# Kernel tuning notes

Hardware: AMD Instinct MI355X
Metric: run time of the kernel (lower is better)

## Reference

```python
import jax, jax.numpy as jnp
import numpy as np

D_MODEL = 1024
NUM_HEADS = 16
HEAD_DIM = D_MODEL // NUM_HEADS
SEQ_LEN = 2048
THETA = 10000.0


def setup_inputs() -> dict:
    key = jax.random.key(0)
    ks = jax.random.split(key, 9)
    s = 1.0 / np.sqrt(D_MODEL)
    inp = {
        "x": jax.random.normal(ks[0], (2, SEQ_LEN, D_MODEL), dtype=jnp.float32),
        "Wq": jax.random.uniform(ks[1], (D_MODEL, D_MODEL), jnp.float32, -s, s),
        "bq": jax.random.uniform(ks[2], (D_MODEL,), jnp.float32, -s, s),
        "Wk": jax.random.uniform(ks[3], (D_MODEL, D_MODEL), jnp.float32, -s, s),
        "bk": jax.random.uniform(ks[4], (D_MODEL,), jnp.float32, -s, s),
        "Wv": jax.random.uniform(ks[5], (D_MODEL, D_MODEL), jnp.float32, -s, s),
        "bv": jax.random.uniform(ks[6], (D_MODEL,), jnp.float32, -s, s),
        "Wo": jax.random.uniform(ks[7], (D_MODEL, D_MODEL), jnp.float32, -s, s),
        "bo": jax.random.uniform(ks[8], (D_MODEL,), jnp.float32, -s, s),
    }
    return inp


def _rope_cos_sin(seq_len, dim, theta):
    inv_freq = 1.0 / theta ** (jnp.arange(0, dim, 2, dtype=jnp.float32) / dim)  # [dim/2]
    t = jnp.arange(seq_len, dtype=jnp.float32)
    freqs = jnp.outer(t, inv_freq)  # [S, dim/2]
    return jnp.cos(freqs), jnp.sin(freqs)


def _apply_rope(x, cos, sin):
    # x: [B, H, S, head_dim]; interleaved complex pairs (even, odd)
    x2 = x.reshape(*x.shape[:-1], -1, 2)  # [B,H,S,hd/2,2]
    xe, xo = x2[..., 0], x2[..., 1]
    c = cos[None, None, :, :]
    s = sin[None, None, :, :]
    oe = xe * c - xo * s
    oo = xe * s + xo * c
    return jnp.stack([oe, oo], axis=-1).reshape(x.shape)


def reference(x, Wq, bq, Wk, bk, Wv, bv, Wo, bo):
    B, S, D = x.shape
    H, hd = NUM_HEADS, HEAD_DIM
    q = x @ Wq.T + bq
    k = x @ Wk.T + bk
    v = x @ Wv.T + bv
    # [B, H, S, hd]
    q = q.reshape(B, S, H, hd).transpose(0, 2, 1, 3)
    k = k.reshape(B, S, H, hd).transpose(0, 2, 1, 3)
    v = v.reshape(B, S, H, hd).transpose(0, 2, 1, 3)
    cos, sin = _rope_cos_sin(S, hd, THETA)
    q = _apply_rope(q, cos, sin)
    k = _apply_rope(k, cos, sin)
    scores = jnp.einsum("bhqd,bhkd->bhqk", q, k) / jnp.sqrt(jnp.float32(hd))
    causal = jnp.triu(jnp.ones((S, S), dtype=bool), k=1)
    scores = jnp.where(causal[None, None, :, :], -jnp.inf, scores)
    attn = jax.nn.softmax(scores, axis=-1)
    out = jnp.einsum("bhqk,bhkd->bhqd", attn, v)
    out = out.transpose(0, 2, 1, 3).reshape(B, S, D)
    return out @ Wo.T + bo
```

## Files before the change

### kernel.cpp

```cpp
#include <hip/hip_runtime.h>
#include <hip/hip_bf16.h>

#define S_LEN 2048
#define DM 1024
#define NH 16
#define HD 64
#define M_ROWS 4096
#define LOG2E 1.4426950408889634f
#define MASKVAL -1.0e4f
#define QSCALE 0.18033688011112042f

typedef __attribute__((ext_vector_type(8))) short short8;
typedef __attribute__((ext_vector_type(2))) float f32x2;
typedef __attribute__((ext_vector_type(4))) float f32x4;
typedef __attribute__((ext_vector_type(16))) float f32x16;

__device__ inline ushort f2b(float f) {
  union { float f; unsigned u; } v; v.f = f;
  unsigned r = v.u + 0x7fffu + ((v.u >> 16) & 1u);
  return (ushort)(r >> 16);
}

__device__ inline float b2f(ushort u) {
  union { unsigned u; float f; } v; v.u = ((unsigned)u) << 16; return v.f;
}

__device__ inline unsigned pk_bf16(float a, float b) {
  __hip_bfloat162 h = __float22bfloat162_rn(make_float2(a, b));
  union { __hip_bfloat162 h; unsigned u; } v; v.h = h;
  return v.u;
}

__device__ inline float fexp2(float x) { return __builtin_amdgcn_exp2f(x); }

__device__ inline void gl_lds16(const void* g, void* l) {
  __builtin_amdgcn_global_load_lds(
      (const __attribute__((address_space(1))) void*)g,
      (__attribute__((address_space(3))) void*)l, 16, 0, 0);
}

__global__ __launch_bounds__(256) void cast_rope_kernel(
    const float* __restrict__ x, const float* __restrict__ Wq, const float* __restrict__ Wk,
    const float* __restrict__ Wv, const float* __restrict__ Wo,
    ushort* __restrict__ xb, ushort* __restrict__ Wqb, ushort* __restrict__ Wkb,
    ushort* __restrict__ Wvb, ushort* __restrict__ Wob,
    float* __restrict__ ropeC, float* __restrict__ ropeS) {
  const int bid = blockIdx.x;
  if (bid >= 8192) {
    int idx = (bid - 8192) * 256 + threadIdx.x;
    int s = idx >> 5, i = idx & 31;
    float inv = exp2f(-(float)i * (13.287712379549449f / 32.0f));
    float a = (float)s * inv;
    ropeC[idx] = cosf(a);
    ropeS[idx] = sinf(a);
    return;
  }
  int i = bid * 256 + threadIdx.x;
  int r = i >> 18, off = i & 0x3FFFF;
  const float4* s;
  uint2* d;
  switch (r) {
    case 0: case 1: case 2: case 3: s = (const float4*)x + i;  d = (uint2*)xb + i;  break;
    case 4: s = (const float4*)Wq + off; d = (uint2*)Wqb + off; break;
    case 5: s = (const float4*)Wk + off; d = (uint2*)Wkb + off; break;
    case 6: s = (const float4*)Wv + off; d = (uint2*)Wvb + off; break;
    default: s = (const float4*)Wo + off; d = (uint2*)Wob + off; break;
  }
  float4 v = *s;
  uint2 o;
  o.x = pk_bf16(v.x, v.y);
  o.y = pk_bf16(v.z, v.w);
  *d = o;
}

__global__ __launch_bounds__(256) void gemm_qkv_kernel(const ushort* __restrict__ xb,
    const ushort* __restrict__ Wqb, const ushort* __restrict__ Wkb, const ushort* __restrict__ Wvb,
    const float* __restrict__ bq, const float* __restrict__ bk, const float* __restrict__ bv,
    const float* __restrict__ ropeC, const float* __restrict__ ropeS,
    ushort* __restrict__ qb, ushort* __restrict__ kb, ushort* __restrict__ vT) {
  __shared__ ushort lds[17408];
  ushort* As = lds;
  ushort* Bs = lds + 8192;
  const int z = blockIdx.z;
  const ushort* W = (z == 0) ? Wqb : ((z == 1) ? Wkb : Wvb);
  const float* bias = (z == 0) ? bq : ((z == 1) ? bk : bv);
  const int m0 = blockIdx.x * 128, n0 = blockIdx.y * 128;
  const int t = threadIdx.x, lane = t & 63, wave = t >> 6;
  const int wr = (wave >> 1) * 64, wc = (wave & 1) * 64;
  const int lr = lane & 15, lg = lane >> 4;

  const int slot0 = wave * 128 + lane, slot1 = slot0 + 64;
  const int row0 = slot0 >> 2, g0 = (slot0 & 3) ^ (row0 & 3);
  const int row1 = slot1 >> 2, g1 = (slot1 & 3) ^ (row1 & 3);
  const ushort* Ap0 = &xb[(size_t)(m0 + row0) * DM + g0 * 8];
  const ushort* Ap1 = &xb[(size_t)(m0 + row1) * DM + g1 * 8];
  const ushort* Wp0 = &W[(size_t)(n0 + row0) * DM + g0 * 8];
  const ushort* Wp1 = &W[(size_t)(n0 + row1) * DM + g1 * 8];

  f32x4 acc[4][4];
#pragma unroll
  for (int a = 0; a < 4; a++)
#pragma unroll
    for (int b = 0; b < 4; b++) acc[a][b] = (f32x4){0.f, 0.f, 0.f, 0.f};

  gl_lds16(Ap0, &As[slot0 * 8]);
  gl_lds16(Ap1, &As[slot1 * 8]);
  gl_lds16(Wp0, &Bs[slot0 * 8]);
  gl_lds16(Wp1, &Bs[slot1 * 8]);
  __syncthreads();

  int buf = 0;
  for (int i = 0; i < 32; i++) {
    if (i + 1 < 32) {
      const int k0 = (i + 1) * 32;
      const int bo = (buf ^ 1) * 4096;
      gl_lds16(Ap0 + k0, &As[bo + slot0 * 8]);
      gl_lds16(Ap1 + k0, &As[bo + slot1 * 8]);
      gl_lds16(Wp0 + k0, &Bs[bo + slot0 * 8]);
      gl_lds16(Wp1 + k0, &Bs[bo + slot1 * 8]);
    }
    const int fb = buf * 4096;
    short8 af[4], bf[4];
#pragma unroll
    for (int mt = 0; mt < 4; mt++) {
      const int row = wr + mt * 16 + lr;
      af[mt] = *(const short8*)&As[fb + (row * 4 + (lg ^ (row & 3))) * 8];
    }
#pragma unroll
    for (int nt = 0; nt < 4; nt++) {
      const int row = wc + nt * 16 + lr;
      bf[nt] = *(const short8*)&Bs[fb + (row * 4 + (lg ^ (row & 3))) * 8];
    }
#pragma unroll
    for (int mt = 0; mt < 4; mt++)
#pragma unroll
      for (int nt = 0; nt < 4; nt++)
        acc[mt][nt] = __builtin_amdgcn_mfma_f32_16x16x32_bf16(af[mt], bf[nt], acc[mt][nt], 0, 0, 0);
    __syncthreads();
    buf ^= 1;
  }

#pragma unroll
  for (int mt = 0; mt < 4; mt++) {
#pragma unroll
    for (int nt = 0; nt < 4; nt++) {
      const int nloc = wc + nt * 16 + lr;
      const float bn = bias[n0 + nloc];
#pragma unroll
      for (int r = 0; r < 4; r++) {
        const int mloc = wr + mt * 16 + lg * 4 + r;
        const ushort v = f2b(acc[mt][nt][r] + bn);
        if (z < 2) lds[mloc * 136 + nloc] = v;
        else       lds[nloc * 136 + mloc] = v;
      }
    }
  }
  __syncthreads();

  const int b = m0 >> 11;
  if (z < 2) {
    ushort* dst = (z == 0) ? qb : kb;
    const float qscale = (z == 0) ? QSCALE : 1.0f;
#pragma unroll
    for (int c = 0; c < 8; c++) {
      const int sloc = c * 16 + (t >> 4);
      const int nloc = (t & 15) * 8;
      short8 val = *(const short8*)&lds[sloc * 136 + nloc];
      const int s = (m0 + sloc) & (S_LEN - 1);
      const int h = (n0 + nloc) >> 6;
      const int d0 = nloc & 63;
      const float4 cv = *(const float4*)&ropeC[s * 32 + d0 / 2];
      const float4 sv = *(const float4*)&ropeS[s * 32 + d0 / 2];
      uint4 o;
      {
        float e = b2f((ushort)val[0]), od = b2f((ushort)val[1]);
        o.x = pk_bf16((e * cv.x - od * sv.x) * qscale, (e * sv.x + od * cv.x) * qscale);
      }
      {
        float e = b2f((ushort)val[2]), od = b2f((ushort)val[3]);
        o.y = pk_bf16((e * cv.y - od * sv.y) * qscale, (e * sv.y + od * cv.y) * qscale);
      }
      {
        float e = b2f((ushort)val[4]), od = b2f((ushort)val[5]);
        o.z = pk_bf16((e * cv.z - od * sv.z) * qscale, (e * sv.z + od * cv.z) * qscale);
      }
      {
        float e = b2f((ushort)val[6]), od = b2f((ushort)val[7]);
        o.w = pk_bf16((e * cv.w - od * sv.w) * qscale, (e * sv.w + od * cv.w) * qscale);
      }
      *(uint4*)&dst[(((size_t)b * NH + h) * S_LEN + s) * HD + d0] = o;
    }
  } else {
    const int sbase = m0 & (S_LEN - 1);
#pragma unroll
    for (int c = 0; c < 8; c++) {
      const int nloc = c * 16 + (t >> 4);
      const int s0 = (t & 15) * 8;
      short8 val = *(const short8*)&lds[nloc * 136 + s0];
      const int h = (n0 + nloc) >> 6;
      const int d = nloc & 63;
      *(short8*)&vT[(((size_t)b * NH + h) * HD + d) * S_LEN + sbase + s0] = val;
    }
  }
}

__global__ __launch_bounds__(256) void flash_kernel(const ushort* __restrict__ qb,
                                                    const ushort* __restrict__ kb,
                                                    const ushort* __restrict__ vT,
                                                    ushort* __restrict__ Oh,
                                                    float* __restrict__ lsum) {
  __shared__ ushort lds[16384];
  const int t = threadIdx.x, lane = t & 63, wave = t >> 6;
  const int q31 = lane & 31, h = lane >> 5;
  const int bh = blockIdx.y;
  const int cid = blockIdx.x;
  const int g = (cid >= 24) ? 3 : (cid >= 12) ? 2 : (cid >= 4) ? 1 : 0;
  const int nc = g + 1;
  const int o = cid - 4 * ((g * (g + 1)) >> 1);
  const int qi = o / nc;
  const int c = o - qi * nc;
  const int qt = g * 4 + qi;
  const int q0 = qt * 128;
  const int ntiles = 2 * qt + 2;
  const int kstart = c * 8;
  const int kend = min(kstart + 8, ntiles);
  const int pidx = bh * 40 + cid;

  const ushort* kbh = kb + (size_t)bh * S_LEN * HD;
  const ushort* vbh = vT + (size_t)bh * HD * S_LEN;

  const int qrow = q0 + wave * 32 + q31;
  const ushort* qptr = qb + ((size_t)bh * S_LEN + qrow) * HD + h * 8;
  short8 qf[4];
#pragma unroll
  for (int s = 0; s < 4; s++) qf[s] = *(const short8*)(qptr + s * 16);

  const int slot0 = wave * 128 + lane, slot1 = slot0 + 64;
  const int row0 = slot0 >> 3, g0 = (slot0 & 7) ^ (row0 & 7);
  const int row1 = slot1 >> 3, g1 = (slot1 & 7) ^ (row1 & 7);
  const int lo0 = wave * 128 * 8, lo1 = lo0 + 64 * 8;

  int foff[4][2];
#pragma unroll
  for (int s = 0; s < 4; s++)
#pragma unroll
    for (int st = 0; st < 2; st++) {
      const int row = st * 32 + q31;
      foff[s][st] = (row * 8 + ((2 * s + h) ^ (row & 7))) * 8;
    }

  {
    const int k00 = kstart * 64;
    gl_lds16(kbh + (size_t)(k00 + row0) * HD + g0 * 8, &lds[0 + lo0]);
    gl_lds16(kbh + (size_t)(k00 + row1) * HD + g1 * 8, &lds[0 + lo1]);
    gl_lds16(vbh + (size_t)row0 * S_LEN + k00 + g0 * 8, &lds[8192 + lo0]);
    gl_lds16(vbh + (size_t)row1 * S_LEN + k00 + g1 * 8, &lds[8192 + lo1]);
  }
  const ushort* kp0 = kbh + (size_t)(kstart * 64 + 64 + row0) * HD + g0 * 8;
  const ushort* kp1 = kbh + (size_t)(kstart * 64 + 64 + row1) * HD + g1 * 8;
  const ushort* vp0 = vbh + (size_t)row0 * S_LEN + kstart * 64 + 64 + g0 * 8;
  const ushort* vp1 = vbh + (size_t)row1 * S_LEN + kstart * 64 + 64 + g1 * 8;
  __syncthreads();

  f32x16 O[2];
#pragma unroll
  for (int st = 0; st < 2; st++)
#pragma unroll
    for (int r = 0; r < 16; r++) O[st][r] = 0.f;

  f32x16 zc;
#pragma unroll
  for (int r = 0; r < 16; r++) zc[r] = 0.f;

  f32x2 lpA = (f32x2){0.f, 0.f}, lpB = (f32x2){0.f, 0.f};

#define FLASH_BODY(KO, VO, PKO, PVO, KT, PREF)                                      \
  {                                                                                 \
    if (PREF) {                                                                     \
      gl_lds16(kp0, &lds[(PKO) + lo0]);                                             \
      gl_lds16(kp1, &lds[(PKO) + lo1]);                                             \
      gl_lds16(vp0, &lds[(PVO) + lo0]);                                             \
      gl_lds16(vp1, &lds[(PVO) + lo1]);                                             \
      kp0 += 64 * HD; kp1 += 64 * HD; vp0 += 64; vp1 += 64;                         \
    }                                                                               \
    f32x16 sc0, sc1;                                                                \
    __builtin_amdgcn_s_setprio(1);                                                  \
    sc0 = __builtin_amdgcn_mfma_f32_32x32x16_bf16(                                  \
        *(const short8*)&lds[(KO) + foff[0][0]], qf[0], zc, 0, 0, 0);               \
    sc1 = __builtin_amdgcn_mfma_f32_32x32x16_bf16(                                  \
        *(const short8*)&lds[(KO) + foff[0][1]], qf[0], zc, 0, 0, 0);               \
    _Pragma("unroll")                                                               \
    for (int s = 1; s < 4; s++) {                                                   \
      sc0 = __builtin_amdgcn_mfma_f32_32x32x16_bf16(                                \
          *(const short8*)&lds[(KO) + foff[s][0]], qf[s], sc0, 0, 0, 0);            \
      sc1 = __builtin_amdgcn_mfma_f32_32x32x16_bf16(                                \
          *(const short8*)&lds[(KO) + foff[s][1]], qf[s], sc1, 0, 0, 0);            \
    }                                                                               \
    __builtin_amdgcn_s_setprio(0);                                                  \
    if ((KT) * 64 + 63 > q0 + wave * 32) {                                          \
      _Pragma("unroll")                                                             \
      for (int r = 0; r < 16; r++) {                                                \
        const int kc0 = (KT) * 64 + (r & 3) + 8 * (r >> 2) + 4 * h;                 \
        if (kc0 > qrow) sc0[r] = MASKVAL;                                           \
        if (kc0 + 32 > qrow) sc1[r] = MASKVAL;                                      \
      }                                                                             \
    }                                                                               \
    _Pragma("unroll")                                                               \
    for (int r = 0; r < 16; r += 2) {                                               \
      const float a0 = fexp2(sc0[r]), a1 = fexp2(sc0[r + 1]);                       \
      const float b0 = fexp2(sc1[r]), b1 = fexp2(sc1[r + 1]);                       \
      sc0[r] = a0; sc0[r + 1] = a1;                                                 \
      sc1[r] = b0; sc1[r + 1] = b1;                                                 \
      lpA += (f32x2){a0, a1};                                                       \
      lpB += (f32x2){b0, b1};                                                       \
    }                                                                               \
    unsigned pp[8][2];                                                              \
    _Pragma("unroll")                                                               \
    for (int rg = 0; rg < 4; rg++) {                                                \
      pp[rg][0] = pk_bf16(sc0[4 * rg + 0], sc0[4 * rg + 1]);                        \
      pp[rg][1] = pk_bf16(sc0[4 * rg + 2], sc0[4 * rg + 3]);                        \
      pp[4 + rg][0] = pk_bf16(sc1[4 * rg + 0], sc1[4 * rg + 1]);                    \
      pp[4 + rg][1] = pk_bf16(sc1[4 * rg + 2], sc1[4 * rg + 3]);                    \
    }                                                                               \
    __builtin_amdgcn_s_setprio(1);                                                  \
    _Pragma("unroll")                                                               \
    for (int s = 0; s < 4; s++) {                                                   \
      unsigned d0 = pp[2 * s][0], e0 = pp[2 * s + 1][0];                            \
      unsigned d1 = pp[2 * s][1], e1 = pp[2 * s + 1][1];                            \
      asm("v_permlane32_swap_b32 %0, %1" : "+v"(d0), "+v"(e0));                     \
      asm("v_permlane32_swap_b32 %0, %1" : "+v"(d1), "+v"(e1));                     \
      union { unsigned u[4]; short8 v; } pf;                                        \
      pf.u[0] = d0;                                                                 \
      pf.u[1] = d1;                                                                 \
      pf.u[2] = e0;                                                                 \
      pf.u[3] = e1;                                                                 \
      O[0] = __builtin_amdgcn_mfma_f32_32x32x16_bf16(                               \
          *(const short8*)&lds[(VO) + foff[s][0]], pf.v, O[0], 0, 0, 0);            \
      O[1] = __builtin_amdgcn_mfma_f32_32x32x16_bf16(                               \
          *(const short8*)&lds[(VO) + foff[s][1]], pf.v, O[1], 0, 0, 0);            \
    }                                                                               \
    __builtin_amdgcn_s_setprio(0);                                                  \
    __syncthreads();                                                                \
  }

  for (int kt = kstart; kt < kend; kt += 2) {
    FLASH_BODY(0, 8192, 4096, 12288, kt, true);
    FLASH_BODY(4096, 12288, 0, 8192, kt + 1, (kt + 2 < kend));
  }
#undef FLASH_BODY

  float lacc = (lpA[0] + lpA[1]) + (lpB[0] + lpB[1]);
  lacc += __shfl_xor(lacc, 32);

  ushort* obase = Oh + ((size_t)pidx * 128 + wave * 32 + q31) * HD;
#pragma unroll
  for (int st = 0; st < 2; st++)
#pragma unroll
    for (int rg = 0; rg < 4; rg++) {
      const int d0 = st * 32 + 8 * rg + 4 * h;
      uint2 w;
      w.x = pk_bf16(O[st][4 * rg + 0], O[st][4 * rg + 1]);
      w.y = pk_bf16(O[st][4 * rg + 2], O[st][4 * rg + 3]);
      *(uint2*)&obase[d0] = w;
    }
  if (h == 0) lsum[(size_t)pidx * 128 + wave * 32 + q31] = lacc;
}

__global__ __launch_bounds__(256) void combine_kernel(const ushort* __restrict__ Oh,
                                                      const float* __restrict__ lsum,
                                                      ushort* __restrict__ attn) {
  const int tid = blockIdx.x * 256 + threadIdx.x;
  const int d8 = tid & 7;
  const int q = (tid >> 3) & (S_LEN - 1);
  const int bh = tid >> 14;
  const int qt = q >> 7, row = q & 127;
  const int g = qt >> 2, nc = g + 1;
  const int base = 4 * ((g * (g + 1)) >> 1) + (qt & 3) * nc;
  const int p0 = bh * 40 + base;

  float l = 0.f;
  float acc[8];
#pragma unroll
  for (int j = 0; j < 8; j++) acc[j] = 0.f;
  for (int c = 0; c < nc; c++) {
    const size_t rowidx = (size_t)(p0 + c) * 128 + row;
    l += lsum[rowidx];
    const uint4 a = *(const uint4*)&Oh[rowidx * HD + d8 * 8];
    const unsigned au[4] = {a.x, a.y, a.z, a.w};
#pragma unroll
    for (int j = 0; j < 4; j++) {
      acc[2 * j] += b2f((ushort)(au[j] & 0xffff));
      acc[2 * j + 1] += b2f((ushort)(au[j] >> 16));
    }
  }
  const float inv = 1.f / l;
  uint4 o;
  unsigned* op = (unsigned*)&o;
#pragma unroll
  for (int j = 0; j < 4; j++) op[j] = pk_bf16(acc[2 * j] * inv, acc[2 * j + 1] * inv);
  const int b = bh >> 4, hh = bh & 15;
  *(uint4*)&attn[((size_t)b * S_LEN + q) * DM + hh * HD + d8 * 8] = o;
}

__global__ __launch_bounds__(256) void gemm_out_kernel(const ushort* __restrict__ attn,
                                                       const ushort* __restrict__ Wob,
                                                       const float* __restrict__ bo,
                                                       float* __restrict__ out) {
  __shared__ ushort As[2][4096];
  __shared__ ushort Bs[2][2048];
  const int m0 = blockIdx.x * 128, n0 = blockIdx.y * 64;
  const int t = threadIdx.x, lane = t & 63, wave = t >> 6;
  const int wm = (wave >> 1) * 64, wn = (wave & 1) * 32;
  const int lr = lane & 15, lg = lane >> 4;
  const int slotA0 = wave * 128 + lane, slotA1 = slotA0 + 64;
  const int rowA0 = slotA0 >> 2, gA0 = (slotA0 & 3) ^ (rowA0 & 3);
  const int rowA1 = slotA1 >> 2, gA1 = (slotA1 & 3) ^ (rowA1 & 3);
  const int slotB = wave * 64 + lane;
  const int rowB = slotB >> 2, gB = (slotB & 3) ^ (rowB & 3);
  const ushort* Ap0 = &attn[(size_t)(m0 + rowA0) * DM + gA0 * 8];
  const ushort* Ap1 = &attn[(size_t)(m0 + rowA1) * DM + gA1 * 8];
  const ushort* Wp  = &Wob[(size_t)(n0 + rowB) * DM + gB * 8];

  f32x4 acc[4][2];
#pragma unroll
  for (int a = 0; a < 4; a++)
#pragma unroll
    for (int b = 0; b < 2; b++) acc[a][b] = (f32x4){0.f, 0.f, 0.f, 0.f};

  gl_lds16(Ap0, &As[0][slotA0 * 8]);
  gl_lds16(Ap1, &As[0][slotA1 * 8]);
  gl_lds16(Wp, &Bs[0][slotB * 8]);
  __syncthreads();

  int buf = 0;
  for (int i = 0; i < 32; i++) {
    if (i + 1 < 32) {
      const int k0 = (i + 1) * 32;
      gl_lds16(Ap0 + k0, &As[buf ^ 1][slotA0 * 8]);
      gl_lds16(Ap1 + k0, &As[buf ^ 1][slotA1 * 8]);
      gl_lds16(Wp + k0, &Bs[buf ^ 1][slotB * 8]);
    }
    short8 af[4], bf[2];
#pragma unroll
    for (int mt = 0; mt < 4; mt++) {
      const int row = wm + mt * 16 + lr;
      af[mt] = *(const short8*)&As[buf][(row * 4 + (lg ^ (row & 3))) * 8];
    }
#pragma unroll
    for (int nt = 0; nt < 2; nt++) {
      const int row = wn + nt * 16 + lr;
      bf[nt] = *(const short8*)&Bs[buf][(row * 4 + (lg ^ (row & 3))) * 8];
    }
#pragma unroll
    for (int mt = 0; mt < 4; mt++)
#pragma unroll
      for (int nt = 0; nt < 2; nt++)
        acc[mt][nt] = __builtin_amdgcn_mfma_f32_16x16x32_bf16(af[mt], bf[nt], acc[mt][nt], 0, 0, 0);
    __syncthreads();
    buf ^= 1;
  }

#pragma unroll
  for (int mt = 0; mt < 4; mt++) {
#pragma unroll
    for (int nt = 0; nt < 2; nt++) {
      const int n = n0 + wn + nt * 16 + lr;
      const float bn = bo[n];
#pragma unroll
      for (int r = 0; r < 4; r++) {
        const int m = m0 + wm + mt * 16 + lg * 4 + r;
        out[(size_t)m * DM + n] = acc[mt][nt][r] + bn;
      }
    }
  }
}

extern "C" void kernel_launch(void* const* d_in, const int* in_sizes, int n_in,
                              void* d_out, int out_size, void* d_ws, size_t ws_size,
                              hipStream_t stream) {
  const float* x  = (const float*)d_in[0];
  const float* Wq = (const float*)d_in[1];
  const float* bq = (const float*)d_in[2];
  const float* Wk = (const float*)d_in[3];
  const float* bk = (const float*)d_in[4];
  const float* Wv = (const float*)d_in[5];
  const float* bv = (const float*)d_in[6];
  const float* Wo = (const float*)d_in[7];
  const float* bo = (const float*)d_in[8];
  float* out = (float*)d_out;

  char* ws = (char*)d_ws;
  size_t off = 0;
  auto alloc = [&](size_t bytes) { char* p = ws + off; off += (bytes + 255) & ~255ull; return p; };
  ushort* xb   = (ushort*)alloc((size_t)M_ROWS * DM * 2);
  ushort* Wqb  = (ushort*)alloc((size_t)DM * DM * 2);
  ushort* Wkb  = (ushort*)alloc((size_t)DM * DM * 2);
  ushort* Wvb  = (ushort*)alloc((size_t)DM * DM * 2);
  ushort* Wob  = (ushort*)alloc((size_t)DM * DM * 2);
  ushort* qb   = (ushort*)alloc((size_t)M_ROWS * DM * 2);
  ushort* kb   = (ushort*)alloc((size_t)M_ROWS * DM * 2);
  ushort* vTb  = (ushort*)alloc((size_t)M_ROWS * DM * 2);
  ushort* attn = (ushort*)alloc((size_t)M_ROWS * DM * 2);
  ushort* Ohb  = (ushort*)alloc((size_t)1280 * 128 * HD * 2);
  float* lsb   = (float*)alloc((size_t)1280 * 128 * 4);
  float* ropeC = (float*)alloc((size_t)S_LEN * 32 * 4);
  float* ropeS = (float*)alloc((size_t)S_LEN * 32 * 4);
  (void)ws_size; (void)in_sizes; (void)n_in; (void)out_size;

  cast_rope_kernel<<<8448, 256, 0, stream>>>(x, Wq, Wk, Wv, Wo, xb, Wqb, Wkb, Wvb, Wob,
                                             ropeC, ropeS);
  gemm_qkv_kernel<<<dim3(M_ROWS / 128, DM / 128, 3), 256, 0, stream>>>(
      xb, Wqb, Wkb, Wvb, bq, bk, bv, ropeC, ropeS, qb, kb, vTb);
  flash_kernel<<<dim3(40, 32), 256, 0, stream>>>(qb, kb, vTb, Ohb, lsb);
  combine_kernel<<<2048, 256, 0, stream>>>(Ohb, lsb, attn);
  gemm_out_kernel<<<dim3(M_ROWS / 128, DM / 64), 256, 0, stream>>>(attn, Wob, bo, out);
}
```

Measured before the change: 190.7 us.

## Double flash query tile to 256 rows per block for K/V reuse

Each wave now handles 64 query rows (two 32-row halves) instead of 32, so each block covers 256 queries and reuses every loaded K/V tile across twice as many rows. The split-K work partition is rebuilt for 8 query tiles (20 blocks per head instead of 40), and the combine kernel indexing and workspace sizes are updated to match. Launch bounds now ask for 3 blocks per CU. In exchange the kernel holds twice as many accumulator and Q registers and launches half as many blocks, which may hurt occupancy and load balance.

```diff
diff --git a/kernel.cpp b/kernel.cpp
--- a/kernel.cpp
+++ b/kernel.cpp
@@ -204,36 +204,40 @@
   }
 }
 
-__global__ __launch_bounds__(256) void flash_kernel(const ushort* __restrict__ qb,
-                                                    const ushort* __restrict__ kb,
-                                                    const ushort* __restrict__ vT,
-                                                    ushort* __restrict__ Oh,
-                                                    float* __restrict__ lsum) {
+__global__ __launch_bounds__(256, 3) void flash_kernel(const ushort* __restrict__ qb,
+                                                       const ushort* __restrict__ kb,
+                                                       const ushort* __restrict__ vT,
+                                                       ushort* __restrict__ Oh,
+                                                       float* __restrict__ lsum) {
   __shared__ ushort lds[16384];
   const int t = threadIdx.x, lane = t & 63, wave = t >> 6;
   const int q31 = lane & 31, h = lane >> 5;
   const int bh = blockIdx.y;
   const int cid = blockIdx.x;
-  const int g = (cid >= 24) ? 3 : (cid >= 12) ? 2 : (cid >= 4) ? 1 : 0;
-  const int nc = g + 1;
-  const int o = cid - 4 * ((g * (g + 1)) >> 1);
-  const int qi = o / nc;
-  const int c = o - qi * nc;
-  const int qt = g * 4 + qi;
-  const int q0 = qt * 128;
-  const int ntiles = 2 * qt + 2;
+  int qt, c;
+  if (cid < 2)       { qt = cid; c = 0; }
+  else if (cid < 6)  { qt = 2 + ((cid - 2) >> 1); c = (cid - 2) & 1; }
+  else if (cid < 12) { const int u = cid - 6; const int w = (u >= 3) ? 1 : 0; qt = 4 + w; c = u - 3 * w; }
+  else               { qt = 6 + ((cid - 12) >> 2); c = (cid - 12) & 3; }
+  const int q0 = qt * 256;
+  const int ntiles = 4 * qt + 4;
   const int kstart = c * 8;
   const int kend = min(kstart + 8, ntiles);
-  const int pidx = bh * 40 + cid;
+  const int pidx = bh * 20 + cid;
 
   const ushort* kbh = kb + (size_t)bh * S_LEN * HD;
   const ushort* vbh = vT + (size_t)bh * HD * S_LEN;
 
-  const int qrow = q0 + wave * 32 + q31;
-  const ushort* qptr = qb + ((size_t)bh * S_LEN + qrow) * HD + h * 8;
-  short8 qf[4];
-#pragma unroll
-  for (int s = 0; s < 4; s++) qf[s] = *(const short8*)(qptr + s * 16);
+  short8 qf[8];
+  {
+    const ushort* qp0 = qb + ((size_t)bh * S_LEN + q0 + wave * 64 + q31) * HD + h * 8;
+    const ushort* qp1 = qp0 + 32 * HD;
+#pragma unroll
+    for (int s = 0; s < 4; s++) {
+      qf[s]     = *(const short8*)(qp0 + s * 16);
+      qf[4 + s] = *(const short8*)(qp1 + s * 16);
+    }
+  }
 
   const int slot0 = wave * 128 + lane, slot1 = slot0 + 64;
   const int row0 = slot0 >> 3, g0 = (slot0 & 7) ^ (row0 & 7);
@@ -262,17 +266,64 @@
   const ushort* vp1 = vbh + (size_t)row1 * S_LEN + kstart * 64 + 64 + g1 * 8;
   __syncthreads();
 
-  f32x16 O[2];
-#pragma unroll
-  for (int st = 0; st < 2; st++)
+  f32x16 O[4];
+#pragma unroll
+  for (int st = 0; st < 4; st++)
 #pragma unroll
     for (int r = 0; r < 16; r++) O[st][r] = 0.f;
 
-  f32x16 zc;
-#pragma unroll
-  for (int r = 0; r < 16; r++) zc[r] = 0.f;
-
-  f32x2 lpA = (f32x2){0.f, 0.f}, lpB = (f32x2){0.f, 0.f};
+  f32x2 lacc0 = (f32x2){0.f, 0.f}, lacc1 = (f32x2){0.f, 0.f};
+
+#define QH_PHASE(KO, VO, KT, QH, QFBASE, LPACC)                                     \
+  {                                                                                 \
+    f32x16 sc0, sc1;                                                                \
+    _Pragma("unroll") for (int r = 0; r < 16; r++) { sc0[r] = 0.f; sc1[r] = 0.f; }  \
+    __builtin_amdgcn_s_setprio(1);                                                  \
+    _Pragma("unroll")                                                               \
+    for (int s = 0; s < 4; s++) {                                                   \
+      sc0 = __builtin_amdgcn_mfma_f32_32x32x16_bf16(                                \
+          *(const short8*)&lds[(KO) + foff[s][0]], qf[(QFBASE) + s], sc0, 0, 0, 0); \
+      sc1 = __builtin_amdgcn_mfma_f32_32x32x16_bf16(                                \
+          *(const short8*)&lds[(KO) + foff[s][1]], qf[(QFBASE) + s], sc1, 0, 0, 0); \
+    }                                                                               \
+    __builtin_amdgcn_s_setprio(0);                                                  \
+    if ((KT) * 64 + 63 > q0 + wave * 64 + (QH) * 32) {                              \
+      const int qr = q0 + wave * 64 + (QH) * 32 + q31;                              \
+      _Pragma("unroll") for (int r = 0; r < 16; r++) {                              \
+        const int kc0 = (KT) * 64 + (r & 3) + 8 * (r >> 2) + 4 * h;                 \
+        if (kc0 > qr) sc0[r] = MASKVAL;                                             \
+        if (kc0 + 32 > qr) sc1[r] = MASKVAL;                                        \
+      }                                                                             \
+    }                                                                               \
+    _Pragma("unroll") for (int r = 0; r < 16; r += 2) {                             \
+      const float a0 = fexp2(sc0[r]), a1 = fexp2(sc0[r + 1]);                       \
+      const float b0 = fexp2(sc1[r]), b1 = fexp2(sc1[r + 1]);                       \
+      sc0[r] = a0; sc0[r + 1] = a1;                                                 \
+      sc1[r] = b0; sc1[r + 1] = b1;                                                 \
+      (LPACC) += (f32x2){a0 + b0, a1 + b1};                                         \
+    }                                                                               \
+    unsigned pp[8][2];                                                              \
+    _Pragma("unroll") for (int rg = 0; rg < 4; rg++) {                              \
+      pp[rg][0] = pk_bf16(sc0[4 * rg + 0], sc0[4 * rg + 1]);                        \
+      pp[rg][1] = pk_bf16(sc0[4 * rg + 2], sc0[4 * rg + 3]);                        \
+      pp[4 + rg][0] = pk_bf16(sc1[4 * rg + 0], sc1[4 * rg + 1]);                    \
+      pp[4 + rg][1] = pk_bf16(sc1[4 * rg + 2], sc1[4 * rg + 3]);                    \
+    }                                                                               \
+    __builtin_amdgcn_s_setprio(1);                                                  \
+    _Pragma("unroll") for (int s = 0; s < 4; s++) {                                 \
+      unsigned d0 = pp[2 * s][0], e0 = pp[2 * s + 1][0];                            \
+      unsigned d1 = pp[2 * s][1], e1 = pp[2 * s + 1][1];                            \
+      asm("v_permlane32_swap_b32 %0, %1" : "+v"(d0), "+v"(e0));                     \
+      asm("v_permlane32_swap_b32 %0, %1" : "+v"(d1), "+v"(e1));                     \
+      union { unsigned u[4]; short8 v; } pf;                                        \
+      pf.u[0] = d0; pf.u[1] = d1; pf.u[2] = e0; pf.u[3] = e1;                       \
+      O[(QH) * 2 + 0] = __builtin_amdgcn_mfma_f32_32x32x16_bf16(                    \
+          *(const short8*)&lds[(VO) + foff[s][0]], pf.v, O[(QH) * 2 + 0], 0, 0, 0); \
+      O[(QH) * 2 + 1] = __builtin_amdgcn_mfma_f32_32x32x16_bf16(                    \
+          *(const short8*)&lds[(VO) + foff[s][1]], pf.v, O[(QH) * 2 + 1], 0, 0, 0); \
+    }                                                                               \
+    __builtin_amdgcn_s_setprio(0);                                                  \
+  }
 
 #define FLASH_BODY(KO, VO, PKO, PVO, KT, PREF)                                      \
   {                                                                                 \
@@ -283,63 +334,8 @@
       gl_lds16(vp1, &lds[(PVO) + lo1]);                                             \
       kp0 += 64 * HD; kp1 += 64 * HD; vp0 += 64; vp1 += 64;                         \
     }                                                                               \
-    f32x16 sc0, sc1;                                                                \
-    __builtin_amdgcn_s_setprio(1);                                                  \
-    sc0 = __builtin_amdgcn_mfma_f32_32x32x16_bf16(                                  \
-        *(const short8*)&lds[(KO) + foff[0][0]], qf[0], zc, 0, 0, 0);               \
-    sc1 = __builtin_amdgcn_mfma_f32_32x32x16_bf16(                                  \
-        *(const short8*)&lds[(KO) + foff[0][1]], qf[0], zc, 0, 0, 0);               \
-    _Pragma("unroll")                                                               \
-    for (int s = 1; s < 4; s++) {                                                   \
-      sc0 = __builtin_amdgcn_mfma_f32_32x32x16_bf16(                                \
-          *(const short8*)&lds[(KO) + foff[s][0]], qf[s], sc0, 0, 0, 0);            \
-      sc1 = __builtin_amdgcn_mfma_f32_32x32x16_bf16(                                \
-          *(const short8*)&lds[(KO) + foff[s][1]], qf[s], sc1, 0, 0, 0);            \
-    }                                                                               \
-    __builtin_amdgcn_s_setprio(0);                                                  \
-    if ((KT) * 64 + 63 > q0 + wave * 32) {                                          \
-      _Pragma("unroll")                                                             \
-      for (int r = 0; r < 16; r++) {                                                \
-        const int kc0 = (KT) * 64 + (r & 3) + 8 * (r >> 2) + 4 * h;                 \
-        if (kc0 > qrow) sc0[r] = MASKVAL;                                           \
-        if (kc0 + 32 > qrow) sc1[r] = MASKVAL;                                      \
-      }                                                                             \
-    }                                                                               \
-    _Pragma("unroll")                                                               \
-    for (int r = 0; r < 16; r += 2) {                                               \
-      const float a0 = fexp2(sc0[r]), a1 = fexp2(sc0[r + 1]);                       \
-      const float b0 = fexp2(sc1[r]), b1 = fexp2(sc1[r + 1]);                       \
-      sc0[r] = a0; sc0[r + 1] = a1;                                                 \
-      sc1[r] = b0; sc1[r + 1] = b1;                                                 \
-      lpA += (f32x2){a0, a1};                                                       \
-      lpB += (f32x2){b0, b1};                                                       \
-    }                                                                               \
-    unsigned pp[8][2];                                                              \
-    _Pragma("unroll")                                                               \
-    for (int rg = 0; rg < 4; rg++) {                                                \
-      pp[rg][0] = pk_bf16(sc0[4 * rg + 0], sc0[4 * rg + 1]);                        \
-      pp[rg][1] = pk_bf16(sc0[4 * rg + 2], sc0[4 * rg + 3]);                        \
-      pp[4 + rg][0] = pk_bf16(sc1[4 * rg + 0], sc1[4 * rg + 1]);                    \
-      pp[4 + rg][1] = pk_bf16(sc1[4 * rg + 2], sc1[4 * rg + 3]);                    \
-    }                                                                               \
-    __builtin_amdgcn_s_setprio(1);                                                  \
-    _Pragma("unroll")                                                               \
-    for (int s = 0; s < 4; s++) {                                                   \
-      unsigned d0 = pp[2 * s][0], e0 = pp[2 * s + 1][0];                            \
-      unsigned d1 = pp[2 * s][1], e1 = pp[2 * s + 1][1];                            \
-      asm("v_permlane32_swap_b32 %0, %1" : "+v"(d0), "+v"(e0));                     \
-      asm("v_permlane32_swap_b32 %0, %1" : "+v"(d1), "+v"(e1));                     \
-      union { unsigned u[4]; short8 v; } pf;                                        \
-      pf.u[0] = d0;                                                                 \
-      pf.u[1] = d1;                                                                 \
-      pf.u[2] = e0;                                                                 \
-      pf.u[3] = e1;                                                                 \
-      O[0] = __builtin_amdgcn_mfma_f32_32x32x16_bf16(                               \
-          *(const short8*)&lds[(VO) + foff[s][0]], pf.v, O[0], 0, 0, 0);            \
-      O[1] = __builtin_amdgcn_mfma_f32_32x32x16_bf16(                               \
-          *(const short8*)&lds[(VO) + foff[s][1]], pf.v, O[1], 0, 0, 0);            \
-    }                                                                               \
-    __builtin_amdgcn_s_setprio(0);                                                  \
+    QH_PHASE(KO, VO, KT, 0, 0, lacc0)                                               \
+    QH_PHASE(KO, VO, KT, 1, 4, lacc1)                                               \
     __syncthreads();                                                                \
   }
 
@@ -348,22 +344,31 @@
     FLASH_BODY(4096, 12288, 0, 8192, kt + 1, (kt + 2 < kend));
   }
 #undef FLASH_BODY
-
-  float lacc = (lpA[0] + lpA[1]) + (lpB[0] + lpB[1]);
-  lacc += __shfl_xor(lacc, 32);
-
-  ushort* obase = Oh + ((size_t)pidx * 128 + wave * 32 + q31) * HD;
-#pragma unroll
-  for (int st = 0; st < 2; st++)
-#pragma unroll
-    for (int rg = 0; rg < 4; rg++) {
-      const int d0 = st * 32 + 8 * rg + 4 * h;
-      uint2 w;
-      w.x = pk_bf16(O[st][4 * rg + 0], O[st][4 * rg + 1]);
-      w.y = pk_bf16(O[st][4 * rg + 2], O[st][4 * rg + 3]);
-      *(uint2*)&obase[d0] = w;
-    }
-  if (h == 0) lsum[(size_t)pidx * 128 + wave * 32 + q31] = lacc;
+#undef QH_PHASE
+
+  float lA = lacc0[0] + lacc0[1];
+  float lB = lacc1[0] + lacc1[1];
+  lA += __shfl_xor(lA, 32);
+  lB += __shfl_xor(lB, 32);
+
+#pragma unroll
+  for (int qh = 0; qh < 2; qh++) {
+    ushort* obase = Oh + ((size_t)pidx * 256 + wave * 64 + qh * 32 + q31) * HD;
+#pragma unroll
+    for (int st = 0; st < 2; st++)
+#pragma unroll
+      for (int rg = 0; rg < 4; rg++) {
+        const int d0 = st * 32 + 8 * rg + 4 * h;
+        uint2 w;
+        w.x = pk_bf16(O[qh * 2 + st][4 * rg + 0], O[qh * 2 + st][4 * rg + 1]);
+        w.y = pk_bf16(O[qh * 2 + st][4 * rg + 2], O[qh * 2 + st][4 * rg + 3]);
+        *(uint2*)&obase[d0] = w;
+      }
+  }
+  if (h == 0) {
+    lsum[(size_t)pidx * 256 + wave * 64 + q31] = lA;
+    lsum[(size_t)pidx * 256 + wave * 64 + 32 + q31] = lB;
+  }
 }
 
 __global__ __launch_bounds__(256) void combine_kernel(const ushort* __restrict__ Oh,
@@ -373,17 +378,17 @@
   const int d8 = tid & 7;
   const int q = (tid >> 3) & (S_LEN - 1);
   const int bh = tid >> 14;
-  const int qt = q >> 7, row = q & 127;
-  const int g = qt >> 2, nc = g + 1;
-  const int base = 4 * ((g * (g + 1)) >> 1) + (qt & 3) * nc;
-  const int p0 = bh * 40 + base;
+  const int qt = q >> 8, row = q & 255;
+  const int nc = (qt >> 1) + 1;
+  const int base = ((qt + 1) * (qt + 1)) >> 2;
+  const int p0 = bh * 20 + base;
 
   float l = 0.f;
   float acc[8];
 #pragma unroll
   for (int j = 0; j < 8; j++) acc[j] = 0.f;
   for (int c = 0; c < nc; c++) {
-    const size_t rowidx = (size_t)(p0 + c) * 128 + row;
+    const size_t rowidx = (size_t)(p0 + c) * 256 + row;
     l += lsum[rowidx];
     const uint4 a = *(const uint4*)&Oh[rowidx * HD + d8 * 8];
     const unsigned au[4] = {a.x, a.y, a.z, a.w};
@@ -501,8 +506,8 @@
   ushort* kb   = (ushort*)alloc((size_t)M_ROWS * DM * 2);
   ushort* vTb  = (ushort*)alloc((size_t)M_ROWS * DM * 2);
   ushort* attn = (ushort*)alloc((size_t)M_ROWS * DM * 2);
-  ushort* Ohb  = (ushort*)alloc((size_t)1280 * 128 * HD * 2);
-  float* lsb   = (float*)alloc((size_t)1280 * 128 * 4);
+  ushort* Ohb  = (ushort*)alloc((size_t)640 * 256 * HD * 2);
+  float* lsb   = (float*)alloc((size_t)640 * 256 * 4);
   float* ropeC = (float*)alloc((size_t)S_LEN * 32 * 4);
   float* ropeS = (float*)alloc((size_t)S_LEN * 32 * 4);
   (void)ws_size; (void)in_sizes; (void)n_in; (void)out_size;
@@ -511,7 +516,7 @@
                                              ropeC, ropeS);
   gemm_qkv_kernel<<<dim3(M_ROWS / 128, DM / 128, 3), 256, 0, stream>>>(
       xb, Wqb, Wkb, Wvb, bq, bk, bv, ropeC, ropeS, qb, kb, vTb);
-  flash_kernel<<<dim3(40, 32), 256, 0, stream>>>(qb, kb, vTb, Ohb, lsb);
+  flash_kernel<<<dim3(20, 32), 256, 0, stream>>>(qb, kb, vTb, Ohb, lsb);
   combine_kernel<<<2048, 256, 0, stream>>>(Ohb, lsb, attn);
   gemm_out_kernel<<<dim3(M_ROWS / 128, DM / 64), 256, 0, stream>>>(attn, Wob, bo, out);
 }
```

Result: slower. 287.7 us (+50.9%).
